# Optimization experiments

Measured on AMD Instinct MI355X. Metric: run time of the kernel, lower is better.

The kernel has to match this reference:

```python
import jax, jax.numpy as jnp
import numpy as np

B, S, H = 4096, 50, 256

def setup_inputs() -> dict:
    key = jax.random.key(0)
    k = jax.random.split(key, 6)
    scale = 1.0 / np.sqrt(H)
    return {
        "C": jax.random.normal(k[0], (B, S, H), dtype=jnp.float32),
        "G": jax.random.uniform(k[1], (B, S), dtype=jnp.float32),
        "W_ih": jax.random.normal(k[2], (3 * H, H), dtype=jnp.float32) * scale,
        "W_hh": jax.random.normal(k[3], (3 * H, H), dtype=jnp.float32) * scale,
        "b_ih": jax.random.normal(k[4], (3 * H,), dtype=jnp.float32) * scale,
        "b_hh": jax.random.normal(k[5], (3 * H,), dtype=jnp.float32) * scale,
    }

def _gru_gated_scan(C, G, W_ih, W_hh, b_ih, b_hh):
    hidden = W_hh.shape[1]
    # precompute input-side gate pre-activations for all steps: [B,S,3H]
    gi_all = jnp.einsum('bsh,gh->bsg', C, W_ih) + b_ih

    def step(h, inputs):
        # h: [B,H]; gi: [B,3H]; g: [B]
        gi, g = inputs
        gh = h @ W_hh.T + b_hh  # [B,3H]
        i_r, i_z, i_n = jnp.split(gi, 3, axis=-1)
        h_r, h_z, h_n = jnp.split(gh, 3, axis=-1)
        r = jax.nn.sigmoid(i_r + h_r)
        z = jax.nn.sigmoid(i_z + h_z)
        n = jnp.tanh(i_n + r * h_n)
        h_new = (1.0 - z) * n + z * h  # PyTorch GRU update
        g = g[:, None]
        h_out = g * h_new + (1.0 - g) * h  # gated memory blend
        return h_out, None

    h0 = jnp.zeros((C.shape[0], hidden), dtype=C.dtype)
    # scan over sentence dim
    h_final, _ = jax.lax.scan(
        step, h0, (jnp.swapaxes(gi_all, 0, 1), jnp.swapaxes(G, 0, 1)))
    return h_final[:, None, :]  # [B,1,H], matches h.transpose(0,1)

def reference(C, G, W_ih, W_hh, b_ih, b_hh):
    return _gru_gated_scan(C, G, W_ih, W_hh, b_ih, b_hh)
```

## Files before the change

kernel.cpp:

```cpp
#include <hip/hip_runtime.h>
#include <hip/hip_fp16.h>

typedef _Float16 half8 __attribute__((ext_vector_type(8)));
typedef _Float16 half4 __attribute__((ext_vector_type(4)));
typedef float floatx4 __attribute__((ext_vector_type(4)));

#define BB 4096
#define SS 50
#define HH 256
#define APAD 264

__global__ void cvt_w(const float* __restrict__ wih,
                      const float* __restrict__ whh,
                      _Float16* __restrict__ ws) {
    int idx = (blockIdx.x * 256 + threadIdx.x) * 4;
    const int half1 = 768 * 256;
    const float* src = (idx < half1) ? (wih + idx) : (whh + (idx - half1));
    float4 v = *(const float4*)src;
    half4 h;
    h[0] = (_Float16)v.x; h[1] = (_Float16)v.y;
    h[2] = (_Float16)v.z; h[3] = (_Float16)v.w;
    *(half4*)(ws + idx) = h;
}

__global__ __launch_bounds__(512, 2) void gru_scan(
    const float* __restrict__ C, const float* __restrict__ G,
    const _Float16* __restrict__ Wih, const _Float16* __restrict__ Whh,
    const float* __restrict__ bih, const float* __restrict__ bhh,
    float* __restrict__ out)
{
    __shared__ _Float16 cA[16 * APAD];
    __shared__ _Float16 hA[2][16 * APAD];
    __shared__ float gS[16];

    const int tid  = threadIdx.x;
    const int wave = tid >> 6;
    const int lane = tid & 63;
    const int q    = lane >> 4;
    const int c    = lane & 15;
    const int rb   = blockIdx.x * 16;

    float bi[3][2], bh[3][2];
#pragma unroll
    for (int g = 0; g < 3; ++g)
#pragma unroll
        for (int t = 0; t < 2; ++t) {
            int n = g * 256 + wave * 32 + t * 16 + c;
            bi[g][t] = bih[n];
            bh[g][t] = bhh[n];
        }

    const _Float16* wiP[3][2];
    const _Float16* whP[3][2];
#pragma unroll
    for (int g = 0; g < 3; ++g)
#pragma unroll
        for (int t = 0; t < 2; ++t) {
            int n0 = g * 256 + wave * 32 + t * 16;
            wiP[g][t] = Wih + (size_t)(n0 + c) * HH + q * 8;
            whP[g][t] = Whh + (size_t)(n0 + c) * HH + q * 8;
        }

    float hreg[2][4];
#pragma unroll
    for (int t = 0; t < 2; ++t)
#pragma unroll
        for (int r = 0; r < 4; ++r) hreg[t][r] = 0.f;

    for (int i = tid; i < 16 * APAD; i += 512) hA[0][i] = (_Float16)0.f;
    __syncthreads();

    const int m_st = tid & 15;
    const int ch   = tid >> 4;
    const float* crow = C + (size_t)(rb + m_st) * (SS * HH) + ch * 8;

    for (int s = 0; s < SS; ++s) {
        {
            const float4* p = (const float4*)(crow + (size_t)s * HH);
            float4 v0 = p[0];
            float4 v1 = p[1];
            half8 hv;
            hv[0] = (_Float16)v0.x; hv[1] = (_Float16)v0.y;
            hv[2] = (_Float16)v0.z; hv[3] = (_Float16)v0.w;
            hv[4] = (_Float16)v1.x; hv[5] = (_Float16)v1.y;
            hv[6] = (_Float16)v1.z; hv[7] = (_Float16)v1.w;
            *(half8*)&cA[m_st * APAD + ch * 8] = hv;
            if (tid < 16) gS[tid] = G[(size_t)(rb + tid) * SS + s];
        }
        __syncthreads();

        const _Float16* hAr = hA[s & 1];

        floatx4 acc_i[3][2], acc_h[3][2];
#pragma unroll
        for (int g = 0; g < 3; ++g)
#pragma unroll
            for (int t = 0; t < 2; ++t) {
                acc_i[g][t] = (floatx4){0.f, 0.f, 0.f, 0.f};
                acc_h[g][t] = (floatx4){0.f, 0.f, 0.f, 0.f};
            }

#pragma unroll
        for (int kt = 0; kt < 8; ++kt) {
            half8 aC = *(const half8*)&cA[c * APAD + kt * 32 + q * 8];
            half8 aH = *(const half8*)&hAr[c * APAD + kt * 32 + q * 8];
#pragma unroll
            for (int g = 0; g < 3; ++g)
#pragma unroll
                for (int t = 0; t < 2; ++t) {
                    half8 bI = *(const half8*)(wiP[g][t] + kt * 32);
                    half8 bH = *(const half8*)(whP[g][t] + kt * 32);
                    acc_i[g][t] = __builtin_amdgcn_mfma_f32_16x16x32_f16(aC, bI, acc_i[g][t], 0, 0, 0);
                    acc_h[g][t] = __builtin_amdgcn_mfma_f32_16x16x32_f16(aH, bH, acc_h[g][t], 0, 0, 0);
                }
        }

        _Float16* hAw = hA[(s + 1) & 1];
#pragma unroll
        for (int t = 0; t < 2; ++t)
#pragma unroll
            for (int r = 0; r < 4; ++r) {
                int m = q * 4 + r;
                float ir  = acc_i[0][t][r] + bi[0][t];
                float hr  = acc_h[0][t][r] + bh[0][t];
                float iz  = acc_i[1][t][r] + bi[1][t];
                float hz  = acc_h[1][t][r] + bh[1][t];
                float in_ = acc_i[2][t][r] + bi[2][t];
                float hn  = acc_h[2][t][r] + bh[2][t];
                float rg  = 1.f / (1.f + __expf(-(ir + hr)));
                float zg  = 1.f / (1.f + __expf(-(iz + hz)));
                float pre = in_ + rg * hn;
                float ap  = fabsf(pre);
                float e2  = __expf(-2.f * ap);
                float th  = (1.f - e2) / (1.f + e2);
                float ng  = (pre < 0.f) ? -th : th;
                float hold = hreg[t][r];
                float hnew = (1.f - zg) * ng + zg * hold;
                float gg   = gS[m];
                float hout = gg * hnew + (1.f - gg) * hold;
                hreg[t][r] = hout;
                hAw[m * APAD + wave * 32 + t * 16 + c] = (_Float16)hout;
            }
        __syncthreads();
    }

#pragma unroll
    for (int t = 0; t < 2; ++t)
#pragma unroll
        for (int r = 0; r < 4; ++r) {
            int m = q * 4 + r;
            out[(size_t)(rb + m) * HH + wave * 32 + t * 16 + c] = hreg[t][r];
        }
}

extern "C" void kernel_launch(void* const* d_in, const int* in_sizes, int n_in,
                              void* d_out, int out_size, void* d_ws, size_t ws_size,
                              hipStream_t stream) {
    const float* C   = (const float*)d_in[0];
    const float* G   = (const float*)d_in[1];
    const float* Wih = (const float*)d_in[2];
    const float* Whh = (const float*)d_in[3];
    const float* bih = (const float*)d_in[4];
    const float* bhh = (const float*)d_in[5];
    _Float16* wsh = (_Float16*)d_ws;

    cvt_w<<<384, 256, 0, stream>>>(Wih, Whh, wsh);
    gru_scan<<<BB / 16, 512, 0, stream>>>(C, G, wsh, wsh + 768 * 256,
                                          bih, bhh, (float*)d_out);
}
```

Measured before the change: 1.395 ms.

## Process 32 batch rows per block and prefetch next step's inputs

Each block now handles 32 batch rows instead of 16, so every weight fragment loaded from global memory feeds two MFMAs, halving weight traffic per row. The C and G loads for step s+1 are issued with nontemporal loads right after the barrier, overlapping them with the current step's matrix work. This doubles the accumulator and hidden-state register footprint and lowers launch bounds to one block per CU, leaving only 128 blocks on a 256-CU device, which risks poor occupancy and idle CUs.

```diff
diff --git a/kernel.cpp b/kernel.cpp
--- a/kernel.cpp
+++ b/kernel.cpp
@@ -4,10 +4,12 @@
 typedef _Float16 half8 __attribute__((ext_vector_type(8)));
 typedef _Float16 half4 __attribute__((ext_vector_type(4)));
 typedef float floatx4 __attribute__((ext_vector_type(4)));
+typedef float fvec4 __attribute__((ext_vector_type(4)));
 
 #define BB 4096
 #define SS 50
 #define HH 256
+#define ROWS 32
 #define APAD 264
 
 __global__ void cvt_w(const float* __restrict__ wih,
@@ -16,29 +18,29 @@
     int idx = (blockIdx.x * 256 + threadIdx.x) * 4;
     const int half1 = 768 * 256;
     const float* src = (idx < half1) ? (wih + idx) : (whh + (idx - half1));
-    float4 v = *(const float4*)src;
+    fvec4 v = *(const fvec4*)src;
     half4 h;
     h[0] = (_Float16)v.x; h[1] = (_Float16)v.y;
     h[2] = (_Float16)v.z; h[3] = (_Float16)v.w;
     *(half4*)(ws + idx) = h;
 }
 
-__global__ __launch_bounds__(512, 2) void gru_scan(
+__global__ __launch_bounds__(512, 1) void gru_scan(
     const float* __restrict__ C, const float* __restrict__ G,
     const _Float16* __restrict__ Wih, const _Float16* __restrict__ Whh,
     const float* __restrict__ bih, const float* __restrict__ bhh,
     float* __restrict__ out)
 {
-    __shared__ _Float16 cA[16 * APAD];
-    __shared__ _Float16 hA[2][16 * APAD];
-    __shared__ float gS[16];
+    __shared__ _Float16 cA[ROWS * APAD];
+    __shared__ _Float16 hA[2][ROWS * APAD];
+    __shared__ float gS[ROWS];
 
     const int tid  = threadIdx.x;
     const int wave = tid >> 6;
     const int lane = tid & 63;
     const int q    = lane >> 4;
     const int c    = lane & 15;
-    const int rb   = blockIdx.x * 16;
+    const int rb   = blockIdx.x * ROWS;
 
     float bi[3][2], bh[3][2];
 #pragma unroll
@@ -61,96 +63,133 @@
             whP[g][t] = Whh + (size_t)(n0 + c) * HH + q * 8;
         }
 
-    float hreg[2][4];
-#pragma unroll
-    for (int t = 0; t < 2; ++t)
-#pragma unroll
-        for (int r = 0; r < 4; ++r) hreg[t][r] = 0.f;
-
-    for (int i = tid; i < 16 * APAD; i += 512) hA[0][i] = (_Float16)0.f;
+    float hreg[2][2][4];
+#pragma unroll
+    for (int mt = 0; mt < 2; ++mt)
+#pragma unroll
+        for (int t = 0; t < 2; ++t)
+#pragma unroll
+            for (int r = 0; r < 4; ++r) hreg[mt][t][r] = 0.f;
+
+    for (int i = tid; i < ROWS * APAD; i += 512) hA[0][i] = (_Float16)0.f;
+
+    const int m_st = tid & 31;
+    const int ch   = tid >> 5;
+    const float* crow = C + (size_t)(rb + m_st) * (SS * HH) + ch * 8;
+
+    fvec4 pf0, pf1, pf2, pf3;
+    float gpf = 0.f;
+    {
+        const fvec4* p  = (const fvec4*)(crow);
+        const fvec4* p2 = (const fvec4*)(crow + 128);
+        pf0 = __builtin_nontemporal_load(p);
+        pf1 = __builtin_nontemporal_load(p + 1);
+        pf2 = __builtin_nontemporal_load(p2);
+        pf3 = __builtin_nontemporal_load(p2 + 1);
+        if (tid < ROWS) gpf = __builtin_nontemporal_load(G + (size_t)(rb + tid) * SS);
+    }
     __syncthreads();
-
-    const int m_st = tid & 15;
-    const int ch   = tid >> 4;
-    const float* crow = C + (size_t)(rb + m_st) * (SS * HH) + ch * 8;
 
     for (int s = 0; s < SS; ++s) {
         {
-            const float4* p = (const float4*)(crow + (size_t)s * HH);
-            float4 v0 = p[0];
-            float4 v1 = p[1];
             half8 hv;
-            hv[0] = (_Float16)v0.x; hv[1] = (_Float16)v0.y;
-            hv[2] = (_Float16)v0.z; hv[3] = (_Float16)v0.w;
-            hv[4] = (_Float16)v1.x; hv[5] = (_Float16)v1.y;
-            hv[6] = (_Float16)v1.z; hv[7] = (_Float16)v1.w;
+            hv[0] = (_Float16)pf0.x; hv[1] = (_Float16)pf0.y;
+            hv[2] = (_Float16)pf0.z; hv[3] = (_Float16)pf0.w;
+            hv[4] = (_Float16)pf1.x; hv[5] = (_Float16)pf1.y;
+            hv[6] = (_Float16)pf1.z; hv[7] = (_Float16)pf1.w;
             *(half8*)&cA[m_st * APAD + ch * 8] = hv;
-            if (tid < 16) gS[tid] = G[(size_t)(rb + tid) * SS + s];
+            half8 hw;
+            hw[0] = (_Float16)pf2.x; hw[1] = (_Float16)pf2.y;
+            hw[2] = (_Float16)pf2.z; hw[3] = (_Float16)pf2.w;
+            hw[4] = (_Float16)pf3.x; hw[5] = (_Float16)pf3.y;
+            hw[6] = (_Float16)pf3.z; hw[7] = (_Float16)pf3.w;
+            *(half8*)&cA[m_st * APAD + 128 + ch * 8] = hw;
+            if (tid < ROWS) gS[tid] = gpf;
         }
         __syncthreads();
 
+        if (s + 1 < SS) {
+            const fvec4* p  = (const fvec4*)(crow + (size_t)(s + 1) * HH);
+            const fvec4* p2 = (const fvec4*)(crow + (size_t)(s + 1) * HH + 128);
+            pf0 = __builtin_nontemporal_load(p);
+            pf1 = __builtin_nontemporal_load(p + 1);
+            pf2 = __builtin_nontemporal_load(p2);
+            pf3 = __builtin_nontemporal_load(p2 + 1);
+            if (tid < ROWS) gpf = __builtin_nontemporal_load(G + (size_t)(rb + tid) * SS + s + 1);
+        }
+
         const _Float16* hAr = hA[s & 1];
 
-        floatx4 acc_i[3][2], acc_h[3][2];
+        floatx4 acc_i[3][2][2], acc_h[3][2][2];
 #pragma unroll
         for (int g = 0; g < 3; ++g)
 #pragma unroll
-            for (int t = 0; t < 2; ++t) {
-                acc_i[g][t] = (floatx4){0.f, 0.f, 0.f, 0.f};
-                acc_h[g][t] = (floatx4){0.f, 0.f, 0.f, 0.f};
-            }
+            for (int t = 0; t < 2; ++t)
+#pragma unroll
+                for (int mt = 0; mt < 2; ++mt) {
+                    acc_i[g][t][mt] = (floatx4){0.f, 0.f, 0.f, 0.f};
+                    acc_h[g][t][mt] = (floatx4){0.f, 0.f, 0.f, 0.f};
+                }
 
 #pragma unroll
         for (int kt = 0; kt < 8; ++kt) {
-            half8 aC = *(const half8*)&cA[c * APAD + kt * 32 + q * 8];
-            half8 aH = *(const half8*)&hAr[c * APAD + kt * 32 + q * 8];
+            half8 aC0 = *(const half8*)&cA[(c)      * APAD + kt * 32 + q * 8];
+            half8 aC1 = *(const half8*)&cA[(16 + c) * APAD + kt * 32 + q * 8];
+            half8 aH0 = *(const half8*)&hAr[(c)      * APAD + kt * 32 + q * 8];
+            half8 aH1 = *(const half8*)&hAr[(16 + c) * APAD + kt * 32 + q * 8];
 #pragma unroll
             for (int g = 0; g < 3; ++g)
 #pragma unroll
                 for (int t = 0; t < 2; ++t) {
                     half8 bI = *(const half8*)(wiP[g][t] + kt * 32);
                     half8 bH = *(const half8*)(whP[g][t] + kt * 32);
-                    acc_i[g][t] = __builtin_amdgcn_mfma_f32_16x16x32_f16(aC, bI, acc_i[g][t], 0, 0, 0);
-                    acc_h[g][t] = __builtin_amdgcn_mfma_f32_16x16x32_f16(aH, bH, acc_h[g][t], 0, 0, 0);
+                    acc_i[g][t][0] = __builtin_amdgcn_mfma_f32_16x16x32_f16(aC0, bI, acc_i[g][t][0], 0, 0, 0);
+                    acc_i[g][t][1] = __builtin_amdgcn_mfma_f32_16x16x32_f16(aC1, bI, acc_i[g][t][1], 0, 0, 0);
+                    acc_h[g][t][0] = __builtin_amdgcn_mfma_f32_16x16x32_f16(aH0, bH, acc_h[g][t][0], 0, 0, 0);
+                    acc_h[g][t][1] = __builtin_amdgcn_mfma_f32_16x16x32_f16(aH1, bH, acc_h[g][t][1], 0, 0, 0);
                 }
         }
 
         _Float16* hAw = hA[(s + 1) & 1];
+#pragma unroll
+        for (int mt = 0; mt < 2; ++mt)
+#pragma unroll
+            for (int t = 0; t < 2; ++t)
+#pragma unroll
+                for (int r = 0; r < 4; ++r) {
+                    int m = q * 4 + r;
+                    float ir  = acc_i[0][t][mt][r] + bi[0][t];
+                    float hr  = acc_h[0][t][mt][r] + bh[0][t];
+                    float iz  = acc_i[1][t][mt][r] + bi[1][t];
+                    float hz  = acc_h[1][t][mt][r] + bh[1][t];
+                    float in_ = acc_i[2][t][mt][r] + bi[2][t];
+                    float hn  = acc_h[2][t][mt][r] + bh[2][t];
+                    float rg  = 1.f / (1.f + __expf(-(ir + hr)));
+                    float zg  = 1.f / (1.f + __expf(-(iz + hz)));
+                    float pre = in_ + rg * hn;
+                    float ap  = fabsf(pre);
+                    float e2  = __expf(-2.f * ap);
+                    float th  = (1.f - e2) / (1.f + e2);
+                    float ng  = (pre < 0.f) ? -th : th;
+                    float hold = hreg[mt][t][r];
+                    float hnew = (1.f - zg) * ng + zg * hold;
+                    float gg   = gS[mt * 16 + m];
+                    float hout = gg * hnew + (1.f - gg) * hold;
+                    hreg[mt][t][r] = hout;
+                    hAw[(mt * 16 + m) * APAD + wave * 32 + t * 16 + c] = (_Float16)hout;
+                }
+        __syncthreads();
+    }
+
+#pragma unroll
+    for (int mt = 0; mt < 2; ++mt)
 #pragma unroll
         for (int t = 0; t < 2; ++t)
 #pragma unroll
             for (int r = 0; r < 4; ++r) {
                 int m = q * 4 + r;
-                float ir  = acc_i[0][t][r] + bi[0][t];
-                float hr  = acc_h[0][t][r] + bh[0][t];
-                float iz  = acc_i[1][t][r] + bi[1][t];
-                float hz  = acc_h[1][t][r] + bh[1][t];
-                float in_ = acc_i[2][t][r] + bi[2][t];
-                float hn  = acc_h[2][t][r] + bh[2][t];
-                float rg  = 1.f / (1.f + __expf(-(ir + hr)));
-                float zg  = 1.f / (1.f + __expf(-(iz + hz)));
-                float pre = in_ + rg * hn;
-                float ap  = fabsf(pre);
-                float e2  = __expf(-2.f * ap);
-                float th  = (1.f - e2) / (1.f + e2);
-                float ng  = (pre < 0.f) ? -th : th;
-                float hold = hreg[t][r];
-                float hnew = (1.f - zg) * ng + zg * hold;
-                float gg   = gS[m];
-                float hout = gg * hnew + (1.f - gg) * hold;
-                hreg[t][r] = hout;
-                hAw[m * APAD + wave * 32 + t * 16 + c] = (_Float16)hout;
+                out[(size_t)(rb + mt * 16 + m) * HH + wave * 32 + t * 16 + c] = hreg[mt][t][r];
             }
-        __syncthreads();
-    }
-
-#pragma unroll
-    for (int t = 0; t < 2; ++t)
-#pragma unroll
-        for (int r = 0; r < 4; ++r) {
-            int m = q * 4 + r;
-            out[(size_t)(rb + m) * HH + wave * 32 + t * 16 + c] = hreg[t][r];
-        }
 }
 
 extern "C" void kernel_launch(void* const* d_in, const int* in_sizes, int n_in,
@@ -165,6 +204,6 @@
     _Float16* wsh = (_Float16*)d_ws;
 
     cvt_w<<<384, 256, 0, stream>>>(Wih, Whh, wsh);
-    gru_scan<<<BB / 16, 512, 0, stream>>>(C, G, wsh, wsh + 768 * 256,
-                                          bih, bhh, (float*)d_out);
+    gru_scan<<<BB / ROWS, 512, 0, stream>>>(C, G, wsh, wsh + 768 * 256,
+                                            bih, bhh, (float*)d_out);
 }
```

Result: slower. 1.958 ms (+40.4%).

## Split GRU scan into register-resident W_ih projection and W_hh recurrence phases

Applied to the files above, without the earlier changes.

The fused kernel is restructured into a chunked two-phase scheme. For each chunk of timesteps, W_ih fragments are held in registers while the input projections (with the r/z biases folded in) are computed and written to a global fp16 workspace. W_hh fragments are then loaded into registers and the recurrence runs over the chunk, reading the precomputed projections back. This removes per-step global/L2 weight fragment loads and halves the MFMA work on the serial dependency chain. In exchange it adds workspace traffic, lowers precision by storing gi in fp16, and likely raises register pressure from 48 half8 weight registers per thread. The old fused kernel is kept as a fallback when the workspace is too small.

```diff
diff --git a/kernel.cpp b/kernel.cpp
--- a/kernel.cpp
+++ b/kernel.cpp
@@ -4,26 +4,200 @@
 typedef _Float16 half8 __attribute__((ext_vector_type(8)));
 typedef _Float16 half4 __attribute__((ext_vector_type(4)));
 typedef float floatx4 __attribute__((ext_vector_type(4)));
-
-#define BB 4096
+typedef float fvec4 __attribute__((ext_vector_type(4)));
+
 #define SS 50
 #define HH 256
 #define APAD 264
+#define WHALF (768 * 256)
+
+__device__ __forceinline__ float sigm(float x) { return 1.f / (1.f + __expf(-x)); }
+__device__ __forceinline__ float tanh_f(float x) {
+    float ap = fabsf(x);
+    float e2 = __expf(-2.f * ap);
+    float th = (1.f - e2) / (1.f + e2);
+    return (x < 0.f) ? -th : th;
+}
 
 __global__ void cvt_w(const float* __restrict__ wih,
                       const float* __restrict__ whh,
                       _Float16* __restrict__ ws) {
     int idx = (blockIdx.x * 256 + threadIdx.x) * 4;
-    const int half1 = 768 * 256;
-    const float* src = (idx < half1) ? (wih + idx) : (whh + (idx - half1));
-    float4 v = *(const float4*)src;
+    const float* src = (idx < WHALF) ? (wih + idx) : (whh + (idx - WHALF));
+    fvec4 v = *(const fvec4*)src;
     half4 h;
     h[0] = (_Float16)v.x; h[1] = (_Float16)v.y;
     h[2] = (_Float16)v.z; h[3] = (_Float16)v.w;
     *(half4*)(ws + idx) = h;
 }
 
-__global__ __launch_bounds__(512, 2) void gru_scan(
+__global__ __launch_bounds__(512, 2) void gru_all(
+    const float* __restrict__ C, const float* __restrict__ G,
+    const float* __restrict__ bih, const float* __restrict__ bhh,
+    const _Float16* __restrict__ Wf, _Float16* __restrict__ giws,
+    float* __restrict__ out, int Sc)
+{
+    __shared__ _Float16 cA[2][16 * APAD];
+    __shared__ _Float16 hA[2][16 * APAD];
+
+    const int tid  = threadIdx.x;
+    const int w    = tid >> 6;
+    const int lane = tid & 63;
+    const int q    = lane >> 4;
+    const int c    = lane & 15;
+    const int rb   = blockIdx.x * 16;
+
+    const _Float16* Wih = Wf;
+    const _Float16* Whh = Wf + WHALF;
+
+    float bsum[6], bhn[2];
+#pragma unroll
+    for (int t2 = 0; t2 < 6; ++t2) {
+        int g = t2 >> 1, t = t2 & 1;
+        int n = g * 256 + w * 32 + t * 16 + c;
+        bsum[t2] = bih[n] + (g < 2 ? bhh[n] : 0.f);
+    }
+#pragma unroll
+    for (int t = 0; t < 2; ++t) bhn[t] = bhh[512 + w * 32 + t * 16 + c];
+
+    float hreg[2][4];
+#pragma unroll
+    for (int t = 0; t < 2; ++t)
+#pragma unroll
+        for (int r = 0; r < 4; ++r) hreg[t][r] = 0.f;
+
+    for (int i = tid; i < 16 * APAD; i += 512) hA[0][i] = (_Float16)0.f;
+
+    const int m_st = tid & 15;
+    const int chk  = tid >> 4;
+    const float* crow = C + (size_t)(rb + m_st) * (SS * HH) + chk * 8;
+    _Float16* giB = giws + (size_t)blockIdx.x * Sc * 12288 + tid * 24;
+
+    half8 wf[6][8];
+    int hp = 0;
+    const int nch = (SS + Sc - 1) / Sc;
+
+    for (int cc = 0; cc < nch; ++cc) {
+        const int s0  = cc * Sc;
+        const int Scc = (Sc < SS - s0) ? Sc : (SS - s0);
+
+#pragma unroll
+        for (int t2 = 0; t2 < 6; ++t2) {
+            const _Float16* base = Wih +
+                (size_t)(((t2 >> 1) * 256 + w * 32 + (t2 & 1) * 16) + c) * HH + q * 8;
+#pragma unroll
+            for (int kt = 0; kt < 8; ++kt) wf[t2][kt] = *(const half8*)(base + kt * 32);
+        }
+        fvec4 cf0 = __builtin_nontemporal_load((const fvec4*)(crow + (size_t)s0 * HH));
+        fvec4 cf1 = __builtin_nontemporal_load((const fvec4*)(crow + (size_t)s0 * HH + 4));
+
+        for (int sc = 0; sc < Scc; ++sc) {
+            const int s = s0 + sc;
+            {
+                half8 hv;
+                hv[0] = (_Float16)cf0.x; hv[1] = (_Float16)cf0.y;
+                hv[2] = (_Float16)cf0.z; hv[3] = (_Float16)cf0.w;
+                hv[4] = (_Float16)cf1.x; hv[5] = (_Float16)cf1.y;
+                hv[6] = (_Float16)cf1.z; hv[7] = (_Float16)cf1.w;
+                *(half8*)&cA[sc & 1][m_st * APAD + chk * 8] = hv;
+            }
+            __syncthreads();
+            if (sc + 1 < Scc) {
+                cf0 = __builtin_nontemporal_load((const fvec4*)(crow + (size_t)(s + 1) * HH));
+                cf1 = __builtin_nontemporal_load((const fvec4*)(crow + (size_t)(s + 1) * HH + 4));
+            }
+            floatx4 acc[6];
+#pragma unroll
+            for (int t2 = 0; t2 < 6; ++t2) acc[t2] = (floatx4){0.f, 0.f, 0.f, 0.f};
+#pragma unroll
+            for (int kt = 0; kt < 8; ++kt) {
+                half8 a = *(const half8*)&cA[sc & 1][c * APAD + kt * 32 + q * 8];
+#pragma unroll
+                for (int t2 = 0; t2 < 6; ++t2)
+                    acc[t2] = __builtin_amdgcn_mfma_f32_16x16x32_f16(a, wf[t2][kt], acc[t2], 0, 0, 0);
+            }
+            half8 o[3];
+#pragma unroll
+            for (int t2 = 0; t2 < 6; ++t2)
+#pragma unroll
+                for (int r = 0; r < 4; ++r) {
+                    int idx = t2 * 4 + r;
+                    o[idx >> 3][idx & 7] = (_Float16)(acc[t2][r] + bsum[t2]);
+                }
+            _Float16* gp = giB + (size_t)sc * 12288;
+            *(half8*)gp        = o[0];
+            *(half8*)(gp + 8)  = o[1];
+            *(half8*)(gp + 16) = o[2];
+        }
+
+#pragma unroll
+        for (int t2 = 0; t2 < 6; ++t2) {
+            const _Float16* base = Whh +
+                (size_t)(((t2 >> 1) * 256 + w * 32 + (t2 & 1) * 16) + c) * HH + q * 8;
+#pragma unroll
+            for (int kt = 0; kt < 8; ++kt) wf[t2][kt] = *(const half8*)(base + kt * 32);
+        }
+
+        for (int sc = 0; sc < Scc; ++sc) {
+            const int s = s0 + sc;
+            __syncthreads();
+            const _Float16* gp = giB + (size_t)sc * 12288;
+            half8 g0 = *(const half8*)gp;
+            half8 g1 = *(const half8*)(gp + 8);
+            half8 g2 = *(const half8*)(gp + 16);
+            float gv[4];
+#pragma unroll
+            for (int r = 0; r < 4; ++r) gv[r] = G[(size_t)(rb + q * 4 + r) * SS + s];
+
+            floatx4 acch[6];
+#pragma unroll
+            for (int t2 = 0; t2 < 6; ++t2) acch[t2] = (floatx4){0.f, 0.f, 0.f, 0.f};
+#pragma unroll
+            for (int kt = 0; kt < 8; ++kt) {
+                half8 a = *(const half8*)&hA[hp][c * APAD + kt * 32 + q * 8];
+#pragma unroll
+                for (int t2 = 0; t2 < 6; ++t2)
+                    acch[t2] = __builtin_amdgcn_mfma_f32_16x16x32_f16(a, wf[t2][kt], acch[t2], 0, 0, 0);
+            }
+
+            float gif[24];
+#pragma unroll
+            for (int idx = 0; idx < 24; ++idx)
+                gif[idx] = (float)((idx < 8) ? g0[idx] : (idx < 16) ? g1[idx - 8] : g2[idx - 16]);
+
+            _Float16* hw = hA[hp ^ 1];
+#pragma unroll
+            for (int t = 0; t < 2; ++t)
+#pragma unroll
+                for (int r = 0; r < 4; ++r) {
+                    float i_r = gif[(0 * 2 + t) * 4 + r];
+                    float i_z = gif[(1 * 2 + t) * 4 + r];
+                    float i_n = gif[(2 * 2 + t) * 4 + r];
+                    float h_r = acch[0 * 2 + t][r];
+                    float h_z = acch[1 * 2 + t][r];
+                    float h_n = acch[2 * 2 + t][r] + bhn[t];
+                    float rg = sigm(i_r + h_r);
+                    float zg = sigm(i_z + h_z);
+                    float ng = tanh_f(i_n + rg * h_n);
+                    float hold = hreg[t][r];
+                    float hnew = (1.f - zg) * ng + zg * hold;
+                    float gg = gv[r];
+                    float hout = gg * hnew + (1.f - gg) * hold;
+                    hreg[t][r] = hout;
+                    hw[(q * 4 + r) * APAD + w * 32 + t * 16 + c] = (_Float16)hout;
+                }
+            hp ^= 1;
+        }
+    }
+
+#pragma unroll
+    for (int t = 0; t < 2; ++t)
+#pragma unroll
+        for (int r = 0; r < 4; ++r)
+            out[(size_t)(rb + q * 4 + r) * HH + w * 32 + t * 16 + c] = hreg[t][r];
+}
+
+__global__ __launch_bounds__(512, 2) void gru_fused(
     const float* __restrict__ C, const float* __restrict__ G,
     const _Float16* __restrict__ Wih, const _Float16* __restrict__ Whh,
     const float* __restrict__ bih, const float* __restrict__ bhh,
@@ -32,26 +206,17 @@
     __shared__ _Float16 cA[16 * APAD];
     __shared__ _Float16 hA[2][16 * APAD];
     __shared__ float gS[16];
-
-    const int tid  = threadIdx.x;
-    const int wave = tid >> 6;
-    const int lane = tid & 63;
-    const int q    = lane >> 4;
-    const int c    = lane & 15;
-    const int rb   = blockIdx.x * 16;
-
+    const int tid = threadIdx.x, wave = tid >> 6, lane = tid & 63;
+    const int q = lane >> 4, c = lane & 15, rb = blockIdx.x * 16;
     float bi[3][2], bh[3][2];
 #pragma unroll
     for (int g = 0; g < 3; ++g)
 #pragma unroll
         for (int t = 0; t < 2; ++t) {
             int n = g * 256 + wave * 32 + t * 16 + c;
-            bi[g][t] = bih[n];
-            bh[g][t] = bhh[n];
-        }
-
-    const _Float16* wiP[3][2];
-    const _Float16* whP[3][2];
+            bi[g][t] = bih[n]; bh[g][t] = bhh[n];
+        }
+    const _Float16 *wiP[3][2], *whP[3][2];
 #pragma unroll
     for (int g = 0; g < 3; ++g)
 #pragma unroll
@@ -60,25 +225,19 @@
             wiP[g][t] = Wih + (size_t)(n0 + c) * HH + q * 8;
             whP[g][t] = Whh + (size_t)(n0 + c) * HH + q * 8;
         }
-
     float hreg[2][4];
 #pragma unroll
     for (int t = 0; t < 2; ++t)
 #pragma unroll
         for (int r = 0; r < 4; ++r) hreg[t][r] = 0.f;
-
     for (int i = tid; i < 16 * APAD; i += 512) hA[0][i] = (_Float16)0.f;
     __syncthreads();
-
-    const int m_st = tid & 15;
-    const int ch   = tid >> 4;
+    const int m_st = tid & 15, ch = tid >> 4;
     const float* crow = C + (size_t)(rb + m_st) * (SS * HH) + ch * 8;
-
     for (int s = 0; s < SS; ++s) {
         {
-            const float4* p = (const float4*)(crow + (size_t)s * HH);
-            float4 v0 = p[0];
-            float4 v1 = p[1];
+            fvec4 v0 = *(const fvec4*)(crow + (size_t)s * HH);
+            fvec4 v1 = *(const fvec4*)(crow + (size_t)s * HH + 4);
             half8 hv;
             hv[0] = (_Float16)v0.x; hv[1] = (_Float16)v0.y;
             hv[2] = (_Float16)v0.z; hv[3] = (_Float16)v0.w;
@@ -88,9 +247,7 @@
             if (tid < 16) gS[tid] = G[(size_t)(rb + tid) * SS + s];
         }
         __syncthreads();
-
         const _Float16* hAr = hA[s & 1];
-
         floatx4 acc_i[3][2], acc_h[3][2];
 #pragma unroll
         for (int g = 0; g < 3; ++g)
@@ -99,7 +256,6 @@
                 acc_i[g][t] = (floatx4){0.f, 0.f, 0.f, 0.f};
                 acc_h[g][t] = (floatx4){0.f, 0.f, 0.f, 0.f};
             }
-
 #pragma unroll
         for (int kt = 0; kt < 8; ++kt) {
             half8 aC = *(const half8*)&cA[c * APAD + kt * 32 + q * 8];
@@ -114,43 +270,29 @@
                     acc_h[g][t] = __builtin_amdgcn_mfma_f32_16x16x32_f16(aH, bH, acc_h[g][t], 0, 0, 0);
                 }
         }
-
         _Float16* hAw = hA[(s + 1) & 1];
 #pragma unroll
         for (int t = 0; t < 2; ++t)
 #pragma unroll
             for (int r = 0; r < 4; ++r) {
                 int m = q * 4 + r;
-                float ir  = acc_i[0][t][r] + bi[0][t];
-                float hr  = acc_h[0][t][r] + bh[0][t];
-                float iz  = acc_i[1][t][r] + bi[1][t];
-                float hz  = acc_h[1][t][r] + bh[1][t];
-                float in_ = acc_i[2][t][r] + bi[2][t];
-                float hn  = acc_h[2][t][r] + bh[2][t];
-                float rg  = 1.f / (1.f + __expf(-(ir + hr)));
-                float zg  = 1.f / (1.f + __expf(-(iz + hz)));
-                float pre = in_ + rg * hn;
-                float ap  = fabsf(pre);
-                float e2  = __expf(-2.f * ap);
-                float th  = (1.f - e2) / (1.f + e2);
-                float ng  = (pre < 0.f) ? -th : th;
+                float rg = sigm(acc_i[0][t][r] + bi[0][t] + acc_h[0][t][r] + bh[0][t]);
+                float zg = sigm(acc_i[1][t][r] + bi[1][t] + acc_h[1][t][r] + bh[1][t]);
+                float ng = tanh_f(acc_i[2][t][r] + bi[2][t] + rg * (acc_h[2][t][r] + bh[2][t]));
                 float hold = hreg[t][r];
                 float hnew = (1.f - zg) * ng + zg * hold;
-                float gg   = gS[m];
+                float gg = gS[m];
                 float hout = gg * hnew + (1.f - gg) * hold;
                 hreg[t][r] = hout;
                 hAw[m * APAD + wave * 32 + t * 16 + c] = (_Float16)hout;
             }
         __syncthreads();
     }
-
 #pragma unroll
     for (int t = 0; t < 2; ++t)
 #pragma unroll
-        for (int r = 0; r < 4; ++r) {
-            int m = q * 4 + r;
-            out[(size_t)(rb + m) * HH + wave * 32 + t * 16 + c] = hreg[t][r];
-        }
+        for (int r = 0; r < 4; ++r)
+            out[(size_t)(rb + q * 4 + r) * HH + wave * 32 + t * 16 + c] = hreg[t][r];
 }
 
 extern "C" void kernel_launch(void* const* d_in, const int* in_sizes, int n_in,
@@ -163,8 +305,18 @@
     const float* bih = (const float*)d_in[4];
     const float* bhh = (const float*)d_in[5];
     _Float16* wsh = (_Float16*)d_ws;
+    const size_t wbytes = (size_t)WHALF * 2 * 2;
+    const size_t per_sc = (size_t)256 * 512 * 24 * 2;
+    size_t avail = ws_size > wbytes ? ws_size - wbytes : 0;
+    long Sc_l = (long)(avail / per_sc);
+    int Sc = Sc_l > 50 ? 50 : (int)Sc_l;
 
     cvt_w<<<384, 256, 0, stream>>>(Wih, Whh, wsh);
-    gru_scan<<<BB / 16, 512, 0, stream>>>(C, G, wsh, wsh + 768 * 256,
-                                          bih, bhh, (float*)d_out);
-}
+    if (Sc >= 1) {
+        gru_all<<<256, 512, 0, stream>>>(C, G, bih, bhh, wsh,
+                                         wsh + (size_t)WHALF * 2, (float*)d_out, Sc);
+    } else {
+        gru_fused<<<256, 512, 0, stream>>>(C, G, wsh, wsh + WHALF,
+                                           bih, bhh, (float*)d_out);
+    }
+}
```

Measured after the change: 1.300 ms. 6.8% less time.
